# Kernel tuning notes

Measured on AMD Instinct MI355X. Metric: run time of the kernel, lower is better.

## Reference

```python
import jax, jax.numpy as jnp
import numpy as np

BN_EPS = 1e-5
K_HOPS = 10


def setup_inputs() -> dict:
    key = jax.random.key(0)
    ks = jax.random.split(key, 8)
    N, F, H, C, E = 169343, 128, 256, 40, 1200000
    return {
        "x": jax.random.normal(ks[0], (N, F), dtype=jnp.float32),
        "edge_index": jax.random.randint(ks[1], (2, E), 0, N, dtype=jnp.int64),
        "norm": jax.random.uniform(ks[2], (E,), dtype=jnp.float32),
        "W1": jax.random.normal(ks[3], (F, H), dtype=jnp.float32) * (1.0 / np.sqrt(F)),
        "b1": jnp.zeros((H,), jnp.float32),
        "bn_gamma": jnp.ones((H,), jnp.float32),
        "bn_beta": jnp.zeros((H,), jnp.float32),
        "bn_mean": jnp.zeros((H,), jnp.float32),
        "bn_var": jnp.ones((H,), jnp.float32),
        "W2": jax.random.normal(ks[4], (H, C), dtype=jnp.float32) * (1.0 / np.sqrt(H)),
        "b2": jnp.zeros((C,), jnp.float32),
        "proj_w": jax.random.normal(ks[5], (C,), dtype=jnp.float32) * (1.0 / np.sqrt(C)),
        "proj_b": jnp.zeros((1,), jnp.float32),
    }


def reference(x, edge_index, norm, W1, b1, bn_gamma, bn_beta, bn_mean, bn_var,
              W2, b2, proj_w, proj_b):
    N = x.shape[0]
    src, dst = edge_index[0], edge_index[1]

    # MLP head: Linear -> BatchNorm (eval, running stats) -> ReLU -> Linear
    h = x @ W1 + b1
    h = (h - bn_mean) * jax.lax.rsqrt(bn_var + BN_EPS) * bn_gamma + bn_beta
    h = jax.nn.relu(h)  # dropout: identity at inference
    h = h @ W2 + b2  # [N, C]

    # K-hop norm-weighted scatter-add propagation, collecting snapshots
    def hop(carry, _):
        msgs = norm[:, None] * carry[src]              # [E, C]
        nxt = jax.ops.segment_sum(msgs, dst, num_segments=N)
        return nxt, nxt

    _, hops = jax.lax.scan(hop, h, None, length=K_HOPS)  # [K, N, C]
    pps = jnp.concatenate([h[None], hops], axis=0)       # [K+1, N, C]
    pps = jnp.transpose(pps, (1, 0, 2))                  # [N, K+1, C]

    # sigmoid attention over hops, weighted combine
    retain = jax.nn.sigmoid(pps @ proj_w + proj_b[0])    # [N, K+1]
    out = jnp.einsum("nk,nkc->nc", retain, pps)          # [N, C]
    return jax.nn.log_softmax(out, axis=1)
```

## Files before the change

kernel.cpp:

```cpp
#include <hip/hip_runtime.h>
#include <hip/hip_bf16.h>
#include <math.h>

#define F 128
#define H 256
#define C 40
#define CP 48
#define KHOPS 10
#define TM 32

typedef short bf16x8 __attribute__((ext_vector_type(8)));
typedef float f32x4 __attribute__((ext_vector_type(4)));

__device__ __forceinline__ void split3(float v, ushort& s1, ushort& s2, ushort& s3) {
    unsigned u = __float_as_uint(v);
    float f1 = __uint_as_float(u & 0xFFFF0000u);
    s1 = (ushort)(u >> 16);
    float r = v - f1;
    unsigned ur = __float_as_uint(r);
    float f2 = __uint_as_float(ur & 0xFFFF0000u);
    s2 = (ushort)(ur >> 16);
    float r2 = r - f2;
    s3 = (ushort)(__float_as_uint(r2) >> 16);
}

__global__ void k_count(const int* __restrict__ dst, int E, int* __restrict__ cnt) {
    int e = blockIdx.x * 256 + threadIdx.x;
    if (e < E) atomicAdd(&cnt[dst[e]], 1);
}

__global__ void k_scan1(const int* __restrict__ cnt, int n, int* __restrict__ bsum) {
    __shared__ int sh[256];
    int t = threadIdx.x;
    int base = blockIdx.x * 4096 + t * 16;
    int s = 0;
    for (int i = 0; i < 16; i++) { int idx = base + i; if (idx < n) s += cnt[idx]; }
    sh[t] = s; __syncthreads();
    for (int o = 128; o > 0; o >>= 1) {
        if (t < o) sh[t] += sh[t + o];
        __syncthreads();
    }
    if (t == 0) bsum[blockIdx.x] = sh[0];
}

__global__ void k_scan2(int* __restrict__ bsum, int nb) {
    if (threadIdx.x == 0) {
        int acc = 0;
        for (int i = 0; i < nb; i++) { int v = bsum[i]; bsum[i] = acc; acc += v; }
    }
}

__global__ void k_scan3(const int* __restrict__ cnt, int n, const int* __restrict__ bsum,
                        int* __restrict__ rp) {
    __shared__ int sh[256];
    int t = threadIdx.x;
    int base = blockIdx.x * 4096 + t * 16;
    int local[16]; int s = 0;
    for (int i = 0; i < 16; i++) {
        int idx = base + i;
        int v = (idx < n) ? cnt[idx] : 0;
        local[i] = v; s += v;
    }
    sh[t] = s; __syncthreads();
    for (int o = 1; o < 256; o <<= 1) {
        int v = (t >= o) ? sh[t - o] : 0;
        __syncthreads();
        sh[t] += v;
        __syncthreads();
    }
    int excl = (t == 0) ? 0 : sh[t - 1];
    int run = bsum[blockIdx.x] + excl;
    for (int i = 0; i < 16; i++) {
        int idx = base + i;
        if (idx < n) { rp[idx] = run; run += local[i]; }
    }
}

__global__ void k_fill(const int* __restrict__ src, const int* __restrict__ dst,
                       const float* __restrict__ nrm, int E, const int* __restrict__ rp,
                       int* __restrict__ cur, int2* __restrict__ ep) {
    int e = blockIdx.x * 256 + threadIdx.x;
    if (e < E) {
        int d = dst[e];
        int p = rp[d] + atomicAdd(&cur[d], 1);
        ep[p] = make_int2(src[e], __float_as_int(nrm[e]));
    }
}

__global__ void k_wsplit(const float* __restrict__ W1, ushort* __restrict__ w1a,
                         ushort* __restrict__ w1b, ushort* __restrict__ w1c) {
    int t = blockIdx.x * 256 + threadIdx.x;
    if (t < F * H) {
        int h = t / F, f = t % F;
        ushort a, b, c;
        split3(W1[(size_t)f * H + h], a, b, c);
        w1a[t] = a; w1b[t] = b; w1c[t] = c;
    }
}

__global__ void k_w2split(const float* __restrict__ W2, ushort* __restrict__ w2a,
                          ushort* __restrict__ w2b, ushort* __restrict__ w2c) {
    int t = blockIdx.x * 256 + threadIdx.x;
    if (t < CP * H) {
        int c = t / H, k = t % H;
        float v = (c < C) ? W2[(size_t)k * C + c] : 0.f;
        ushort a, b, cc;
        split3(v, a, b, cc);
        w2a[t] = a; w2b[t] = b; w2c[t] = cc;
    }
}

__launch_bounds__(256, 3)
__global__ void k_mlp(const float* __restrict__ x,
                      const ushort* __restrict__ w1a, const ushort* __restrict__ w1b,
                      const ushort* __restrict__ w1c,
                      const ushort* __restrict__ w2a, const ushort* __restrict__ w2b,
                      const ushort* __restrict__ w2c,
                      const float* __restrict__ b1, const float* __restrict__ g,
                      const float* __restrict__ be, const float* __restrict__ mu,
                      const float* __restrict__ var,
                      const float* __restrict__ b2, const float* __restrict__ pw,
                      const float* __restrict__ pb,
                      float* __restrict__ hbuf, float* __restrict__ oacc, int N) {
    __shared__ float xs[TM][132];
    __shared__ float h1s[TM][260];
    __shared__ float ascS[H], dscS[H];
    __shared__ float sigv[TM];

    int t = threadIdx.x;
    int n0 = blockIdx.x * TM;

    for (int kk = 0; kk < 4; kk++) {
        int idx = kk * 256 + t;
        int node = idx >> 5, f4 = idx & 31;
        int n = n0 + node;
        float4 v = (n < N) ? ((const float4*)x)[(size_t)n * (F / 4) + f4]
                           : make_float4(0.f, 0.f, 0.f, 0.f);
        *((float4*)&xs[node][f4 * 4]) = v;
    }
    {
        float a = g[t] * rsqrtf(var[t] + 1e-5f);
        ascS[t] = a;
        dscS[t] = (b1[t] - mu[t]) * a + be[t];
    }
    __syncthreads();

    int lane = t & 63, wv = t >> 6, quad = lane >> 4, lq = lane & 15;
    int n0w = wv * 64;
    f32x4 acc[2][4];
    #pragma unroll
    for (int mi = 0; mi < 2; mi++)
        #pragma unroll
        for (int ni = 0; ni < 4; ni++)
            acc[mi][ni] = (f32x4){0.f, 0.f, 0.f, 0.f};

    #pragma unroll
    for (int ks = 0; ks < 4; ks++) {
        int k0 = ks * 32 + quad * 8;
        bf16x8 a1[2], a2[2], a3[2];
        #pragma unroll
        for (int mi = 0; mi < 2; mi++) {
            int row = mi * 16 + lq;
            float4 f0 = *((const float4*)&xs[row][k0]);
            float4 f1 = *((const float4*)&xs[row][k0 + 4]);
            float fv[8] = {f0.x, f0.y, f0.z, f0.w, f1.x, f1.y, f1.z, f1.w};
            #pragma unroll
            for (int e = 0; e < 8; e++) {
                ushort sa, sb, sc;
                split3(fv[e], sa, sb, sc);
                a1[mi][e] = (short)sa; a2[mi][e] = (short)sb; a3[mi][e] = (short)sc;
            }
        }
        #pragma unroll
        for (int ni = 0; ni < 4; ni++) {
            size_t wo = (size_t)(n0w + ni * 16 + lq) * F + k0;
            bf16x8 q1 = *((const bf16x8*)(w1a + wo));
            bf16x8 q2 = *((const bf16x8*)(w1b + wo));
            bf16x8 q3 = *((const bf16x8*)(w1c + wo));
            #pragma unroll
            for (int mi = 0; mi < 2; mi++) {
                acc[mi][ni] = __builtin_amdgcn_mfma_f32_16x16x32_bf16(a1[mi], q1, acc[mi][ni], 0, 0, 0);
                acc[mi][ni] = __builtin_amdgcn_mfma_f32_16x16x32_bf16(a1[mi], q2, acc[mi][ni], 0, 0, 0);
                acc[mi][ni] = __builtin_amdgcn_mfma_f32_16x16x32_bf16(a2[mi], q1, acc[mi][ni], 0, 0, 0);
                acc[mi][ni] = __builtin_amdgcn_mfma_f32_16x16x32_bf16(a1[mi], q3, acc[mi][ni], 0, 0, 0);
                acc[mi][ni] = __builtin_amdgcn_mfma_f32_16x16x32_bf16(a2[mi], q2, acc[mi][ni], 0, 0, 0);
                acc[mi][ni] = __builtin_amdgcn_mfma_f32_16x16x32_bf16(a3[mi], q1, acc[mi][ni], 0, 0, 0);
            }
        }
    }

    #pragma unroll
    for (int ni = 0; ni < 4; ni++) {
        int h = n0w + ni * 16 + lq;
        float a = ascS[h], d = dscS[h];
        #pragma unroll
        for (int mi = 0; mi < 2; mi++) {
            #pragma unroll
            for (int r = 0; r < 4; r++) {
                int node = mi * 16 + quad * 4 + r;
                float v = acc[mi][ni][r] * a + d;
                h1s[node][h] = v > 0.f ? v : 0.f;
            }
        }
    }
    __syncthreads();

    f32x4 acc2[2][3];
    #pragma unroll
    for (int mi = 0; mi < 2; mi++)
        #pragma unroll
        for (int ni = 0; ni < 3; ni++)
            acc2[mi][ni] = (f32x4){0.f, 0.f, 0.f, 0.f};

    int kb0 = wv * 64;
    #pragma unroll
    for (int ks2 = 0; ks2 < 2; ks2++) {
        int k0 = kb0 + ks2 * 32 + quad * 8;
        bf16x8 a1[2], a2[2], a3[2];
        #pragma unroll
        for (int mi = 0; mi < 2; mi++) {
            int row = mi * 16 + lq;
            float4 f0 = *((const float4*)&h1s[row][k0]);
            float4 f1 = *((const float4*)&h1s[row][k0 + 4]);
            float fv[8] = {f0.x, f0.y, f0.z, f0.w, f1.x, f1.y, f1.z, f1.w};
            #pragma unroll
            for (int e = 0; e < 8; e++) {
                ushort sa, sb, sc;
                split3(fv[e], sa, sb, sc);
                a1[mi][e] = (short)sa; a2[mi][e] = (short)sb; a3[mi][e] = (short)sc;
            }
        }
        #pragma unroll
        for (int ni = 0; ni < 3; ni++) {
            size_t wo = (size_t)(ni * 16 + lq) * H + k0;
            bf16x8 q1 = *((const bf16x8*)(w2a + wo));
            bf16x8 q2 = *((const bf16x8*)(w2b + wo));
            bf16x8 q3 = *((const bf16x8*)(w2c + wo));
            #pragma unroll
            for (int mi = 0; mi < 2; mi++) {
                acc2[mi][ni] = __builtin_amdgcn_mfma_f32_16x16x32_bf16(a1[mi], q1, acc2[mi][ni], 0, 0, 0);
                acc2[mi][ni] = __builtin_amdgcn_mfma_f32_16x16x32_bf16(a1[mi], q2, acc2[mi][ni], 0, 0, 0);
                acc2[mi][ni] = __builtin_amdgcn_mfma_f32_16x16x32_bf16(a2[mi], q1, acc2[mi][ni], 0, 0, 0);
                acc2[mi][ni] = __builtin_amdgcn_mfma_f32_16x16x32_bf16(a1[mi], q3, acc2[mi][ni], 0, 0, 0);
                acc2[mi][ni] = __builtin_amdgcn_mfma_f32_16x16x32_bf16(a2[mi], q2, acc2[mi][ni], 0, 0, 0);
                acc2[mi][ni] = __builtin_amdgcn_mfma_f32_16x16x32_bf16(a3[mi], q1, acc2[mi][ni], 0, 0, 0);
            }
        }
    }
    __syncthreads();

    float* pbB = &h1s[0][0];
    #pragma unroll
    for (int mi = 0; mi < 2; mi++)
        #pragma unroll
        for (int ni = 0; ni < 3; ni++)
            #pragma unroll
            for (int r = 0; r < 4; r++) {
                int node = mi * 16 + quad * 4 + r;
                int c = ni * 16 + lq;
                pbB[wv * (TM * CP) + node * CP + c] = acc2[mi][ni][r];
            }
    __syncthreads();

    float* hrow = &h1s[0][0] + 4 * TM * CP;
    {
        int ng = t >> 3, cg = t & 7;
        float p = 0.f;
        #pragma unroll
        for (int j = 0; j < 5; j++) {
            int c = cg * 5 + j;
            float h = pbB[0 * (TM * CP) + ng * CP + c]
                    + pbB[1 * (TM * CP) + ng * CP + c]
                    + pbB[2 * (TM * CP) + ng * CP + c]
                    + pbB[3 * (TM * CP) + ng * CP + c] + b2[c];
            hrow[ng * C + c] = h;
            p += h * pw[c];
        }
        #pragma unroll
        for (int m = 1; m < 8; m <<= 1) p += __shfl_xor(p, m);
        if (cg == 0) sigv[ng] = 1.f / (1.f + expf(-(p + pb[0])));
    }
    __syncthreads();

    if (t < 160) {
        int row = t / 5, p = t % 5;
        int n = n0 + row;
        if (n < N) {
            float4 a = *((const float4*)&hrow[row * C + 8 * p]);
            float4 b = *((const float4*)&hrow[row * C + 8 * p + 4]);
            float4* hp = (float4*)(hbuf + (size_t)n * C + 8 * p);
            hp[0] = a; hp[1] = b;
            float sg = sigv[row];
            float4 oa, ob;
            oa.x = sg * a.x; oa.y = sg * a.y; oa.z = sg * a.z; oa.w = sg * a.w;
            ob.x = sg * b.x; ob.y = sg * b.y; ob.z = sg * b.z; ob.w = sg * b.w;
            float4* op = (float4*)(oacc + (size_t)n * C + 8 * p);
            op[0] = oa; op[1] = ob;
        }
    }
}

__global__ void k_hop(const float4* __restrict__ cur4, float4* __restrict__ nxt4,
                      float4* __restrict__ oacc4, const int* __restrict__ rp,
                      const int2* __restrict__ ep,
                      const float* __restrict__ pw, const float* __restrict__ pb,
                      int N, int last) {
    __shared__ float red[320];
    __shared__ float sig[64];
    __shared__ float statm[64];
    __shared__ float stats[64];
    int t = threadIdx.x;
    int nl = t / 5, p = t % 5;
    int n = blockIdx.x * 64 + nl;
    int c0 = 2 * p;
    float4 a0 = make_float4(0.f, 0.f, 0.f, 0.f);
    float4 a1 = make_float4(0.f, 0.f, 0.f, 0.f);
    if (n < N) {
        int b = rp[n], e = rp[n + 1];
        int j = b;
        for (; j + 4 <= e; j += 4) {
            int2 e0 = ep[j], e1 = ep[j + 1], e2 = ep[j + 2], e3 = ep[j + 3];
            const float4* r0 = cur4 + (size_t)e0.x * 10 + c0;
            const float4* r1 = cur4 + (size_t)e1.x * 10 + c0;
            const float4* r2 = cur4 + (size_t)e2.x * 10 + c0;
            const float4* r3 = cur4 + (size_t)e3.x * 10 + c0;
            float4 v00 = r0[0], v01 = r0[1];
            float4 v10 = r1[0], v11 = r1[1];
            float4 v20 = r2[0], v21 = r2[1];
            float4 v30 = r3[0], v31 = r3[1];
            float w0 = __int_as_float(e0.y), w1 = __int_as_float(e1.y);
            float w2 = __int_as_float(e2.y), w3 = __int_as_float(e3.y);
            a0.x += w0 * v00.x; a0.y += w0 * v00.y; a0.z += w0 * v00.z; a0.w += w0 * v00.w;
            a1.x += w0 * v01.x; a1.y += w0 * v01.y; a1.z += w0 * v01.z; a1.w += w0 * v01.w;
            a0.x += w1 * v10.x; a0.y += w1 * v10.y; a0.z += w1 * v10.z; a0.w += w1 * v10.w;
            a1.x += w1 * v11.x; a1.y += w1 * v11.y; a1.z += w1 * v11.z; a1.w += w1 * v11.w;
            a0.x += w2 * v20.x; a0.y += w2 * v20.y; a0.z += w2 * v20.z; a0.w += w2 * v20.w;
            a1.x += w2 * v21.x; a1.y += w2 * v21.y; a1.z += w2 * v21.z; a1.w += w2 * v21.w;
            a0.x += w3 * v30.x; a0.y += w3 * v30.y; a0.z += w3 * v30.z; a0.w += w3 * v30.w;
            a1.x += w3 * v31.x; a1.y += w3 * v31.y; a1.z += w3 * v31.z; a1.w += w3 * v31.w;
        }
        if (j + 2 <= e) {
            int2 e0 = ep[j], e1 = ep[j + 1];
            const float4* r0 = cur4 + (size_t)e0.x * 10 + c0;
            const float4* r1 = cur4 + (size_t)e1.x * 10 + c0;
            float4 v00 = r0[0], v01 = r0[1];
            float4 v10 = r1[0], v11 = r1[1];
            float w0 = __int_as_float(e0.y), w1 = __int_as_float(e1.y);
            a0.x += w0 * v00.x; a0.y += w0 * v00.y; a0.z += w0 * v00.z; a0.w += w0 * v00.w;
            a1.x += w0 * v01.x; a1.y += w0 * v01.y; a1.z += w0 * v01.z; a1.w += w0 * v01.w;
            a0.x += w1 * v10.x; a0.y += w1 * v10.y; a0.z += w1 * v10.z; a0.w += w1 * v10.w;
            a1.x += w1 * v11.x; a1.y += w1 * v11.y; a1.z += w1 * v11.z; a1.w += w1 * v11.w;
            j += 2;
        }
        if (j < e) {
            int2 e0 = ep[j];
            const float4* r0 = cur4 + (size_t)e0.x * 10 + c0;
            float4 v00 = r0[0], v01 = r0[1];
            float w0 = __int_as_float(e0.y);
            a0.x += w0 * v00.x; a0.y += w0 * v00.y; a0.z += w0 * v00.z; a0.w += w0 * v00.w;
            a1.x += w0 * v01.x; a1.y += w0 * v01.y; a1.z += w0 * v01.z; a1.w += w0 * v01.w;
        }
        if (!last) {
            nxt4[(size_t)n * 10 + c0] = a0;
            nxt4[(size_t)n * 10 + c0 + 1] = a1;
        }
    }
    float4 pw0 = ((const float4*)pw)[c0];
    float4 pw1 = ((const float4*)pw)[c0 + 1];
    red[t] = a0.x * pw0.x + a0.y * pw0.y + a0.z * pw0.z + a0.w * pw0.w
           + a1.x * pw1.x + a1.y * pw1.y + a1.z * pw1.z + a1.w * pw1.w;
    __syncthreads();
    if (p == 0) {
        float s = red[t] + red[t + 1] + red[t + 2] + red[t + 3] + red[t + 4];
        sig[nl] = 1.f / (1.f + expf(-(s + pb[0])));
    }
    __syncthreads();
    float4 v0 = make_float4(0.f, 0.f, 0.f, 0.f);
    float4 v1 = make_float4(0.f, 0.f, 0.f, 0.f);
    size_t o = (size_t)n * 10 + c0;
    if (n < N) {
        float sg = sig[nl];
        v0 = oacc4[o]; v1 = oacc4[o + 1];
        v0.x += sg * a0.x; v0.y += sg * a0.y; v0.z += sg * a0.z; v0.w += sg * a0.w;
        v1.x += sg * a1.x; v1.y += sg * a1.y; v1.z += sg * a1.z; v1.w += sg * a1.w;
        if (!last) {
            oacc4[o] = v0;
            oacc4[o + 1] = v1;
        }
    }
    if (last) {
        bool ok = n < N;
        float mx = fmaxf(fmaxf(fmaxf(v0.x, v0.y), fmaxf(v0.z, v0.w)),
                         fmaxf(fmaxf(v1.x, v1.y), fmaxf(v1.z, v1.w)));
        red[t] = ok ? mx : -1e30f;
        __syncthreads();
        if (p == 0) {
            float m = fmaxf(fmaxf(fmaxf(red[t], red[t + 1]), fmaxf(red[t + 2], red[t + 3])),
                            red[t + 4]);
            statm[nl] = m;
        }
        __syncthreads();
        float m = statm[nl];
        float s = 0.f;
        if (ok) {
            s = expf(v0.x - m) + expf(v0.y - m) + expf(v0.z - m) + expf(v0.w - m)
              + expf(v1.x - m) + expf(v1.y - m) + expf(v1.z - m) + expf(v1.w - m);
        }
        red[t] = s;
        __syncthreads();
        if (p == 0) {
            float ssum = red[t] + red[t + 1] + red[t + 2] + red[t + 3] + red[t + 4];
            stats[nl] = logf(ssum);
        }
        __syncthreads();
        if (ok) {
            float ls = statm[nl] + stats[nl];
            oacc4[o]     = make_float4(v0.x - ls, v0.y - ls, v0.z - ls, v0.w - ls);
            oacc4[o + 1] = make_float4(v1.x - ls, v1.y - ls, v1.z - ls, v1.w - ls);
        }
    }
}

extern "C" void kernel_launch(void* const* d_in, const int* in_sizes, int n_in,
                              void* d_out, int out_size, void* d_ws, size_t ws_size,
                              hipStream_t stream) {
    const float* x   = (const float*)d_in[0];
    const int*   ei  = (const int*)d_in[1];
    const float* nrm = (const float*)d_in[2];
    const float* W1  = (const float*)d_in[3];
    const float* b1  = (const float*)d_in[4];
    const float* g   = (const float*)d_in[5];
    const float* be  = (const float*)d_in[6];
    const float* mu  = (const float*)d_in[7];
    const float* var = (const float*)d_in[8];
    const float* W2  = (const float*)d_in[9];
    const float* b2  = (const float*)d_in[10];
    const float* pw  = (const float*)d_in[11];
    const float* pb  = (const float*)d_in[12];
    float* out = (float*)d_out;

    int N = in_sizes[0] / F;
    int E = in_sizes[2];

    char* w = (char*)d_ws;
    auto alloc = [&](size_t bytes) {
        void* p = (void*)w;
        w += ((bytes + 255) / 256) * 256;
        return p;
    };
    int*    rp     = (int*)alloc((size_t)(N + 1) * 4);
    int*    cursor = (int*)alloc((size_t)(N + 1) * 4);
    int*    bsum   = (int*)alloc(1024);
    int2*   ep     = (int2*)alloc((size_t)E * 8);
    ushort* w1a    = (ushort*)alloc((size_t)F * H * 2);
    ushort* w1b    = (ushort*)alloc((size_t)F * H * 2);
    ushort* w1c    = (ushort*)alloc((size_t)F * H * 2);
    ushort* w2a    = (ushort*)alloc((size_t)CP * H * 2);
    ushort* w2b    = (ushort*)alloc((size_t)CP * H * 2);
    ushort* w2c    = (ushort*)alloc((size_t)CP * H * 2);
    float*  bufA   = (float*)alloc((size_t)N * C * 4);
    float*  bufB   = (float*)alloc((size_t)N * C * 4);

    hipMemsetAsync(cursor, 0, (size_t)(N + 1) * 4, stream);

    k_count<<<(E + 255) / 256, 256, 0, stream>>>(ei + E, E, cursor);

    int n1 = N + 1;
    int NB = (n1 + 4095) / 4096;
    k_scan1<<<NB, 256, 0, stream>>>(cursor, n1, bsum);
    k_scan2<<<1, 64, 0, stream>>>(bsum, NB);
    k_scan3<<<NB, 256, 0, stream>>>(cursor, n1, bsum, rp);

    hipMemsetAsync(cursor, 0, (size_t)(N + 1) * 4, stream);
    k_fill<<<(E + 255) / 256, 256, 0, stream>>>(ei, ei + E, nrm, E, rp, cursor, ep);

    k_wsplit<<<(F * H + 255) / 256, 256, 0, stream>>>(W1, w1a, w1b, w1c);
    k_w2split<<<(CP * H + 255) / 256, 256, 0, stream>>>(W2, w2a, w2b, w2c);

    k_mlp<<<(N + TM - 1) / TM, 256, 0, stream>>>(x, w1a, w1b, w1c, w2a, w2b, w2c,
                                                 b1, g, be, mu, var,
                                                 b2, pw, pb, bufA, out, N);

    int nodeBlocks64 = (N + 63) / 64;
    float* cur = bufA;
    float* nxt = bufB;
    for (int k = 0; k < KHOPS; k++) {
        k_hop<<<nodeBlocks64, 320, 0, stream>>>((const float4*)cur, (float4*)nxt, (float4*)out,
                                                rp, ep, pw, pb, N, (k == KHOPS - 1) ? 1 : 0);
        float* tmp = cur; cur = nxt; nxt = tmp;
    }
}
```

Measured before the change: 1.004 ms.

## Pre-split x into bf16 planes in LDS, batch weight loads, deepen gather unroll

In the MLP kernel, x is split into three bf16 planes once while it is staged into shared memory, so the GEMM loop reads bf16x8 operands directly instead of re-splitting floats for every wave. Weight fragments for all N tiles are now loaded before the MFMA chain, and launch bounds drop to 2 blocks per CU. In the propagation kernel, the 4/2/1 unrolled edge loop becomes an 8-wide batched gather with clamped indices and zero weights for the tail, and the oacc load is hoisted ahead of the gather. Together these aim to raise memory-level parallelism in the gather and cut repeated ALU work in the GEMM, at the cost of more registers and lower occupancy.

```diff
diff --git a/kernel.cpp b/kernel.cpp
--- a/kernel.cpp
+++ b/kernel.cpp
@@ -110,7 +110,7 @@
     }
 }
 
-__launch_bounds__(256, 3)
+__launch_bounds__(256, 2)
 __global__ void k_mlp(const float* __restrict__ x,
                       const ushort* __restrict__ w1a, const ushort* __restrict__ w1b,
                       const ushort* __restrict__ w1c,
@@ -122,7 +122,9 @@
                       const float* __restrict__ b2, const float* __restrict__ pw,
                       const float* __restrict__ pb,
                       float* __restrict__ hbuf, float* __restrict__ oacc, int N) {
-    __shared__ float xs[TM][132];
+    __shared__ ushort xsA[TM][136];
+    __shared__ ushort xsB[TM][136];
+    __shared__ ushort xsC[TM][136];
     __shared__ float h1s[TM][260];
     __shared__ float ascS[H], dscS[H];
     __shared__ float sigv[TM];
@@ -136,7 +138,14 @@
         int n = n0 + node;
         float4 v = (n < N) ? ((const float4*)x)[(size_t)n * (F / 4) + f4]
                            : make_float4(0.f, 0.f, 0.f, 0.f);
-        *((float4*)&xs[node][f4 * 4]) = v;
+        ushort4 pa, pm, pc;
+        split3(v.x, pa.x, pm.x, pc.x);
+        split3(v.y, pa.y, pm.y, pc.y);
+        split3(v.z, pa.z, pm.z, pc.z);
+        split3(v.w, pa.w, pm.w, pc.w);
+        *((ushort4*)&xsA[node][f4 * 4]) = pa;
+        *((ushort4*)&xsB[node][f4 * 4]) = pm;
+        *((ushort4*)&xsC[node][f4 * 4]) = pc;
     }
     {
         float a = g[t] * rsqrtf(var[t] + 1e-5f);
@@ -161,30 +170,28 @@
         #pragma unroll
         for (int mi = 0; mi < 2; mi++) {
             int row = mi * 16 + lq;
-            float4 f0 = *((const float4*)&xs[row][k0]);
-            float4 f1 = *((const float4*)&xs[row][k0 + 4]);
-            float fv[8] = {f0.x, f0.y, f0.z, f0.w, f1.x, f1.y, f1.z, f1.w};
-            #pragma unroll
-            for (int e = 0; e < 8; e++) {
-                ushort sa, sb, sc;
-                split3(fv[e], sa, sb, sc);
-                a1[mi][e] = (short)sa; a2[mi][e] = (short)sb; a3[mi][e] = (short)sc;
-            }
-        }
+            a1[mi] = *((const bf16x8*)&xsA[row][k0]);
+            a2[mi] = *((const bf16x8*)&xsB[row][k0]);
+            a3[mi] = *((const bf16x8*)&xsC[row][k0]);
+        }
+        bf16x8 q1[4], q2[4], q3[4];
         #pragma unroll
         for (int ni = 0; ni < 4; ni++) {
             size_t wo = (size_t)(n0w + ni * 16 + lq) * F + k0;
-            bf16x8 q1 = *((const bf16x8*)(w1a + wo));
-            bf16x8 q2 = *((const bf16x8*)(w1b + wo));
-            bf16x8 q3 = *((const bf16x8*)(w1c + wo));
+            q1[ni] = *((const bf16x8*)(w1a + wo));
+            q2[ni] = *((const bf16x8*)(w1b + wo));
+            q3[ni] = *((const bf16x8*)(w1c + wo));
+        }
+        #pragma unroll
+        for (int ni = 0; ni < 4; ni++) {
             #pragma unroll
             for (int mi = 0; mi < 2; mi++) {
-                acc[mi][ni] = __builtin_amdgcn_mfma_f32_16x16x32_bf16(a1[mi], q1, acc[mi][ni], 0, 0, 0);
-                acc[mi][ni] = __builtin_amdgcn_mfma_f32_16x16x32_bf16(a1[mi], q2, acc[mi][ni], 0, 0, 0);
-                acc[mi][ni] = __builtin_amdgcn_mfma_f32_16x16x32_bf16(a2[mi], q1, acc[mi][ni], 0, 0, 0);
-                acc[mi][ni] = __builtin_amdgcn_mfma_f32_16x16x32_bf16(a1[mi], q3, acc[mi][ni], 0, 0, 0);
-                acc[mi][ni] = __builtin_amdgcn_mfma_f32_16x16x32_bf16(a2[mi], q2, acc[mi][ni], 0, 0, 0);
-                acc[mi][ni] = __builtin_amdgcn_mfma_f32_16x16x32_bf16(a3[mi], q1, acc[mi][ni], 0, 0, 0);
+                acc[mi][ni] = __builtin_amdgcn_mfma_f32_16x16x32_bf16(a1[mi], q1[ni], acc[mi][ni], 0, 0, 0);
+                acc[mi][ni] = __builtin_amdgcn_mfma_f32_16x16x32_bf16(a1[mi], q2[ni], acc[mi][ni], 0, 0, 0);
+                acc[mi][ni] = __builtin_amdgcn_mfma_f32_16x16x32_bf16(a2[mi], q1[ni], acc[mi][ni], 0, 0, 0);
+                acc[mi][ni] = __builtin_amdgcn_mfma_f32_16x16x32_bf16(a1[mi], q3[ni], acc[mi][ni], 0, 0, 0);
+                acc[mi][ni] = __builtin_amdgcn_mfma_f32_16x16x32_bf16(a2[mi], q2[ni], acc[mi][ni], 0, 0, 0);
+                acc[mi][ni] = __builtin_amdgcn_mfma_f32_16x16x32_bf16(a3[mi], q1[ni], acc[mi][ni], 0, 0, 0);
             }
         }
     }
@@ -230,20 +237,24 @@
                 a1[mi][e] = (short)sa; a2[mi][e] = (short)sb; a3[mi][e] = (short)sc;
             }
         }
+        bf16x8 q1[3], q2[3], q3[3];
         #pragma unroll
         for (int ni = 0; ni < 3; ni++) {
             size_t wo = (size_t)(ni * 16 + lq) * H + k0;
-            bf16x8 q1 = *((const bf16x8*)(w2a + wo));
-            bf16x8 q2 = *((const bf16x8*)(w2b + wo));
-            bf16x8 q3 = *((const bf16x8*)(w2c + wo));
+            q1[ni] = *((const bf16x8*)(w2a + wo));
+            q2[ni] = *((const bf16x8*)(w2b + wo));
+            q3[ni] = *((const bf16x8*)(w2c + wo));
+        }
+        #pragma unroll
+        for (int ni = 0; ni < 3; ni++) {
             #pragma unroll
             for (int mi = 0; mi < 2; mi++) {
-                acc2[mi][ni] = __builtin_amdgcn_mfma_f32_16x16x32_bf16(a1[mi], q1, acc2[mi][ni], 0, 0, 0);
-                acc2[mi][ni] = __builtin_amdgcn_mfma_f32_16x16x32_bf16(a1[mi], q2, acc2[mi][ni], 0, 0, 0);
-                acc2[mi][ni] = __builtin_amdgcn_mfma_f32_16x16x32_bf16(a2[mi], q1, acc2[mi][ni], 0, 0, 0);
-                acc2[mi][ni] = __builtin_amdgcn_mfma_f32_16x16x32_bf16(a1[mi], q3, acc2[mi][ni], 0, 0, 0);
-                acc2[mi][ni] = __builtin_amdgcn_mfma_f32_16x16x32_bf16(a2[mi], q2, acc2[mi][ni], 0, 0, 0);
-                acc2[mi][ni] = __builtin_amdgcn_mfma_f32_16x16x32_bf16(a3[mi], q1, acc2[mi][ni], 0, 0, 0);
+                acc2[mi][ni] = __builtin_amdgcn_mfma_f32_16x16x32_bf16(a1[mi], q1[ni], acc2[mi][ni], 0, 0, 0);
+                acc2[mi][ni] = __builtin_amdgcn_mfma_f32_16x16x32_bf16(a1[mi], q2[ni], acc2[mi][ni], 0, 0, 0);
+                acc2[mi][ni] = __builtin_amdgcn_mfma_f32_16x16x32_bf16(a2[mi], q1[ni], acc2[mi][ni], 0, 0, 0);
+                acc2[mi][ni] = __builtin_amdgcn_mfma_f32_16x16x32_bf16(a1[mi], q3[ni], acc2[mi][ni], 0, 0, 0);
+                acc2[mi][ni] = __builtin_amdgcn_mfma_f32_16x16x32_bf16(a2[mi], q2[ni], acc2[mi][ni], 0, 0, 0);
+                acc2[mi][ni] = __builtin_amdgcn_mfma_f32_16x16x32_bf16(a3[mi], q1[ni], acc2[mi][ni], 0, 0, 0);
             }
         }
     }
@@ -313,60 +324,45 @@
     int nl = t / 5, p = t % 5;
     int n = blockIdx.x * 64 + nl;
     int c0 = 2 * p;
+    bool ok = n < N;
+    size_t o = (size_t)(ok ? n : 0) * 10 + c0;
+    float4 pw0 = ((const float4*)pw)[c0];
+    float4 pw1 = ((const float4*)pw)[c0 + 1];
+    float4 v0 = make_float4(0.f, 0.f, 0.f, 0.f);
+    float4 v1 = make_float4(0.f, 0.f, 0.f, 0.f);
+    if (ok) { v0 = oacc4[o]; v1 = oacc4[o + 1]; }
     float4 a0 = make_float4(0.f, 0.f, 0.f, 0.f);
     float4 a1 = make_float4(0.f, 0.f, 0.f, 0.f);
-    if (n < N) {
+    if (ok) {
         int b = rp[n], e = rp[n + 1];
-        int j = b;
-        for (; j + 4 <= e; j += 4) {
-            int2 e0 = ep[j], e1 = ep[j + 1], e2 = ep[j + 2], e3 = ep[j + 3];
-            const float4* r0 = cur4 + (size_t)e0.x * 10 + c0;
-            const float4* r1 = cur4 + (size_t)e1.x * 10 + c0;
-            const float4* r2 = cur4 + (size_t)e2.x * 10 + c0;
-            const float4* r3 = cur4 + (size_t)e3.x * 10 + c0;
-            float4 v00 = r0[0], v01 = r0[1];
-            float4 v10 = r1[0], v11 = r1[1];
-            float4 v20 = r2[0], v21 = r2[1];
-            float4 v30 = r3[0], v31 = r3[1];
-            float w0 = __int_as_float(e0.y), w1 = __int_as_float(e1.y);
-            float w2 = __int_as_float(e2.y), w3 = __int_as_float(e3.y);
-            a0.x += w0 * v00.x; a0.y += w0 * v00.y; a0.z += w0 * v00.z; a0.w += w0 * v00.w;
-            a1.x += w0 * v01.x; a1.y += w0 * v01.y; a1.z += w0 * v01.z; a1.w += w0 * v01.w;
-            a0.x += w1 * v10.x; a0.y += w1 * v10.y; a0.z += w1 * v10.z; a0.w += w1 * v10.w;
-            a1.x += w1 * v11.x; a1.y += w1 * v11.y; a1.z += w1 * v11.z; a1.w += w1 * v11.w;
-            a0.x += w2 * v20.x; a0.y += w2 * v20.y; a0.z += w2 * v20.z; a0.w += w2 * v20.w;
-            a1.x += w2 * v21.x; a1.y += w2 * v21.y; a1.z += w2 * v21.z; a1.w += w2 * v21.w;
-            a0.x += w3 * v30.x; a0.y += w3 * v30.y; a0.z += w3 * v30.z; a0.w += w3 * v30.w;
-            a1.x += w3 * v31.x; a1.y += w3 * v31.y; a1.z += w3 * v31.z; a1.w += w3 * v31.w;
-        }
-        if (j + 2 <= e) {
-            int2 e0 = ep[j], e1 = ep[j + 1];
-            const float4* r0 = cur4 + (size_t)e0.x * 10 + c0;
-            const float4* r1 = cur4 + (size_t)e1.x * 10 + c0;
-            float4 v00 = r0[0], v01 = r0[1];
-            float4 v10 = r1[0], v11 = r1[1];
-            float w0 = __int_as_float(e0.y), w1 = __int_as_float(e1.y);
-            a0.x += w0 * v00.x; a0.y += w0 * v00.y; a0.z += w0 * v00.z; a0.w += w0 * v00.w;
-            a1.x += w0 * v01.x; a1.y += w0 * v01.y; a1.z += w0 * v01.z; a1.w += w0 * v01.w;
-            a0.x += w1 * v10.x; a0.y += w1 * v10.y; a0.z += w1 * v10.z; a0.w += w1 * v10.w;
-            a1.x += w1 * v11.x; a1.y += w1 * v11.y; a1.z += w1 * v11.z; a1.w += w1 * v11.w;
-            j += 2;
-        }
-        if (j < e) {
-            int2 e0 = ep[j];
-            const float4* r0 = cur4 + (size_t)e0.x * 10 + c0;
-            float4 v00 = r0[0], v01 = r0[1];
-            float w0 = __int_as_float(e0.y);
-            a0.x += w0 * v00.x; a0.y += w0 * v00.y; a0.z += w0 * v00.z; a0.w += w0 * v00.w;
-            a1.x += w0 * v01.x; a1.y += w0 * v01.y; a1.z += w0 * v01.z; a1.w += w0 * v01.w;
+        for (int j = b; j < e; j += 8) {
+            int cnt = e - j;
+            int2 ee[8];
+            #pragma unroll
+            for (int i = 0; i < 8; i++) {
+                int jj = (i < cnt) ? (j + i) : (e - 1);
+                ee[i] = ep[jj];
+            }
+            float4 va[8], vb[8];
+            #pragma unroll
+            for (int i = 0; i < 8; i++) {
+                const float4* r = cur4 + (size_t)ee[i].x * 10 + c0;
+                va[i] = r[0]; vb[i] = r[1];
+            }
+            #pragma unroll
+            for (int i = 0; i < 8; i++) {
+                float w = (i < cnt) ? __int_as_float(ee[i].y) : 0.f;
+                a0.x += w * va[i].x; a0.y += w * va[i].y;
+                a0.z += w * va[i].z; a0.w += w * va[i].w;
+                a1.x += w * vb[i].x; a1.y += w * vb[i].y;
+                a1.z += w * vb[i].z; a1.w += w * vb[i].w;
+            }
         }
         if (!last) {
-            nxt4[(size_t)n * 10 + c0] = a0;
-            nxt4[(size_t)n * 10 + c0 + 1] = a1;
-        }
-    }
-    float4 pw0 = ((const float4*)pw)[c0];
-    float4 pw1 = ((const float4*)pw)[c0 + 1];
+            nxt4[o] = a0;
+            nxt4[o + 1] = a1;
+        }
+    }
     red[t] = a0.x * pw0.x + a0.y * pw0.y + a0.z * pw0.z + a0.w * pw0.w
            + a1.x * pw1.x + a1.y * pw1.y + a1.z * pw1.z + a1.w * pw1.w;
     __syncthreads();
@@ -375,12 +371,8 @@
         sig[nl] = 1.f / (1.f + expf(-(s + pb[0])));
     }
     __syncthreads();
-    float4 v0 = make_float4(0.f, 0.f, 0.f, 0.f);
-    float4 v1 = make_float4(0.f, 0.f, 0.f, 0.f);
-    size_t o = (size_t)n * 10 + c0;
-    if (n < N) {
+    if (ok) {
         float sg = sig[nl];
-        v0 = oacc4[o]; v1 = oacc4[o + 1];
         v0.x += sg * a0.x; v0.y += sg * a0.y; v0.z += sg * a0.z; v0.w += sg * a0.w;
         v1.x += sg * a1.x; v1.y += sg * a1.y; v1.z += sg * a1.z; v1.w += sg * a1.w;
         if (!last) {
@@ -389,7 +381,6 @@
         }
     }
     if (last) {
-        bool ok = n < N;
         float mx = fmaxf(fmaxf(fmaxf(v0.x, v0.y), fmaxf(v0.z, v0.w)),
                          fmaxf(fmaxf(v1.x, v1.y), fmaxf(v1.z, v1.w)));
         red[t] = ok ? mx : -1e30f;
```

New measurement: 1.076 ms. 7.2% more time.
